# Performance work log

Measured on AMD Instinct MI355X. Metric: run time of the kernel, lower is better.

## Reference

```python
import jax, jax.numpy as jnp
import numpy as np


def conv1x1(x, w, b):
    # x: [B,C,H,W], w: [O,C], b: [O]  (1x1 conv == per-pixel matmul)
    return jnp.einsum('oc,bchw->bohw', w, x) + b[None, :, None, None]


def setup_inputs() -> dict:
    key = jax.random.key(0)
    ks = jax.random.split(key, 8)
    B, C, H, W = 8, 256, 64, 64
    heads, points = 8, 4
    x = jax.random.normal(ks[0], (B, C, H, W), dtype=jnp.float32)
    # small offset weights so sampling grids stay mostly in-range (original inits these to 0)
    w_off = jax.random.normal(ks[1], (heads * points * 2, C), dtype=jnp.float32) * 0.01
    b_off = jax.random.normal(ks[2], (heads * points * 2,), dtype=jnp.float32) * 0.05
    w_attn = jax.random.normal(ks[3], (heads * points, C), dtype=jnp.float32) * 0.02
    b_attn = jnp.full((heads * points,), np.log(1.0 / points), dtype=jnp.float32)
    w_val = jax.random.normal(ks[4], (C, C), dtype=jnp.float32) * (1.0 / np.sqrt(C))
    b_val = jnp.zeros((C,), dtype=jnp.float32)
    w_out = jax.random.normal(ks[5], (C, C), dtype=jnp.float32) * (1.0 / np.sqrt(C))
    b_out = jnp.zeros((C,), dtype=jnp.float32)
    return {"x": x, "w_off": w_off, "b_off": b_off, "w_attn": w_attn, "b_attn": b_attn,
            "w_val": w_val, "b_val": b_val, "w_out": w_out, "b_out": b_out,
            "num_heads": heads, "num_points": points}


def _grid_sample_one(v, g):
    # v: [Cph,H,W] value image; g: [P,H,W,2] sampling grid in [-1,1] (x,y), align_corners=True,
    # bilinear, zero padding. Returns [Cph,P,H,W].
    Cph, H, W = v.shape
    ix = (g[..., 0] + 1.0) * 0.5 * (W - 1)  # [P,H,W]
    iy = (g[..., 1] + 1.0) * 0.5 * (H - 1)
    x0 = jnp.floor(ix); y0 = jnp.floor(iy)
    x1 = x0 + 1.0;      y1 = y0 + 1.0
    wx1 = ix - x0; wx0 = 1.0 - wx1
    wy1 = iy - y0; wy0 = 1.0 - wy1

    def corner(yc, xc, w):
        valid = (xc >= 0) & (xc <= W - 1) & (yc >= 0) & (yc <= H - 1)
        yi = jnp.clip(yc, 0, H - 1).astype(jnp.int32)
        xi = jnp.clip(xc, 0, W - 1).astype(jnp.int32)
        vv = v[:, yi, xi]  # [Cph,P,H,W]
        return vv * (w * valid.astype(w.dtype))[None]

    return (corner(y0, x0, wy0 * wx0) + corner(y0, x1, wy0 * wx1)
            + corner(y1, x0, wy1 * wx0) + corner(y1, x1, wy1 * wx1))


def deformable_attention(x, w_off, b_off, w_attn, b_attn, w_val, b_val, w_out, b_out,
                         num_heads, num_points):
    B, C, H, W = x.shape
    hd, P = num_heads, num_points
    cph = C // hd

    value = conv1x1(x, w_val, b_val)                       # [B,C,H,W]
    offsets = conv1x1(x, w_off, b_off)                     # [B,hd*P*2,H,W]
    attn = conv1x1(x, w_attn, b_attn).reshape(B, hd, P, H, W)
    attn = jax.nn.softmax(attn, axis=2)                    # softmax over points

    gy = jnp.linspace(-1.0, 1.0, H, dtype=x.dtype)
    gx = jnp.linspace(-1.0, 1.0, W, dtype=x.dtype)
    base = jnp.stack(jnp.meshgrid(gx, gy, indexing='xy'), axis=-1)  # [H,W,2] (x,y)

    off = offsets.reshape(B, hd, P, 2, H, W).transpose(0, 1, 2, 4, 5, 3)  # [B,hd,P,H,W,2]
    grid = base[None, None, None] + off                                   # [B,hd,P,H,W,2]

    val = value.reshape(B * hd, cph, H, W)
    grid = grid.reshape(B * hd, P, H, W, 2)
    sampled = jax.vmap(_grid_sample_one)(val, grid)        # [B*hd,cph,P,H,W]
    sampled = sampled.reshape(B, hd, cph, P, H, W)

    weighted = (sampled * attn[:, :, None]).sum(axis=3)    # [B,hd,cph,H,W]
    weighted = weighted.reshape(B, C, H, W)
    return conv1x1(weighted, w_out, b_out) + x


def reference(x, w_off, b_off, w_attn, b_attn, w_val, b_val, w_out, b_out,
              num_heads, num_points):
    return deformable_attention(x, w_off, b_off, w_attn, b_attn, w_val, b_val,
                                w_out, b_out, num_heads, num_points)
```

## Files before the change

### kernel.cpp

```cpp
#include <hip/hip_runtime.h>
#include <cstddef>

#define HW 4096

typedef __attribute__((ext_vector_type(8))) short short8v;
typedef __attribute__((ext_vector_type(4))) float f32x4;

__device__ inline unsigned short f2bf(float f) {
    unsigned int u = __float_as_uint(f);
    u += 0x7FFFu + ((u >> 16) & 1u);
    return (unsigned short)(u >> 16);
}
__device__ inline float bf2f(unsigned short s) {
    return __uint_as_float(((unsigned int)s) << 16);
}

__device__ inline void load_tile(const unsigned short* __restrict__ g, int kc,
                                 int wid, int lane, short8v r[4])
{
    const int s  = lane & 7;
    const int r8 = lane >> 3;
    const unsigned short* src = g + kc + s * 8;
#pragma unroll
    for (int i = 0; i < 4; ++i) {
        const int row = wid * 32 + i * 8 + r8;
        r[i] = *(const short8v*)(src + row * 256);
    }
}

__device__ inline void store_tile(unsigned short* lds, int wid, int lane, const short8v r[4])
{
    const int s  = lane & 7;
    const int r8 = lane >> 3;
#pragma unroll
    for (int i = 0; i < 4; ++i) {
        const int row = wid * 32 + i * 8 + r8;
        *(short8v*)((char*)lds + row * 128 + ((s ^ (row & 7)) << 4)) = r[i];
    }
}

__device__ inline short8v read_frag(const unsigned short* lds, int row, int kbyte, int lane)
{
    const char* p = (const char*)lds + row * 128 + (kbyte ^ ((lane & 7) * 16));
    return *(const short8v*)p;
}

__global__ __launch_bounds__(256)
void prep_kernel(const float* __restrict__ w_off, const float* __restrict__ b_off,
                 const float* __restrict__ w_attn, const float* __restrict__ b_attn,
                 const float* __restrict__ w_val, const float* __restrict__ b_val,
                 const float* __restrict__ w_out,
                 unsigned short* __restrict__ wcat_bf, unsigned short* __restrict__ wauxlo,
                 unsigned short* __restrict__ wout_bf, float* __restrict__ bcat)
{
    int i = blockIdx.x * 256 + threadIdx.x;
    if (i < 384 * 256) {
        int n = i >> 8, k = i & 255;
        float v;
        if (n < 256)      v = w_val[n * 256 + k];
        else if (n < 320) v = w_off[(n - 256) * 256 + k];
        else if (n < 352) v = w_attn[(n - 320) * 256 + k];
        else              v = 0.0f;
        unsigned short hi = f2bf(v);
        wcat_bf[i] = hi;
        if (n >= 256) wauxlo[(n - 256) * 256 + k] = f2bf(v - bf2f(hi));
    }
    if (i < 256 * 256) wout_bf[i] = f2bf(w_out[i]);
    if (i < 512) {
        float v = 0.0f;
        if (i < 256)      v = b_val[i];
        else if (i < 320) v = b_off[i - 256];
        else if (i < 352) v = b_attn[i - 320];
        bcat[i] = v;
    }
}

__global__ __launch_bounds__(256)
void transpose_kernel(const float* __restrict__ x, unsigned short* __restrict__ xhi)
{
    __shared__ float t[64][65];
    const int bid = blockIdx.x;
    const int pt = bid & 63, ct = (bid >> 6) & 3, b = bid >> 8;
    const int tid = threadIdx.x;
    const int rr = tid >> 4, c4 = (tid & 15) * 4;

    const float* src = x + ((size_t)(b * 256 + ct * 64)) * HW + pt * 64;
#pragma unroll
    for (int j = 0; j < 4; ++j) {
        float4 v = *(const float4*)&src[(size_t)(j * 16 + rr) * HW + c4];
        t[j * 16 + rr][c4 + 0] = v.x; t[j * 16 + rr][c4 + 1] = v.y;
        t[j * 16 + rr][c4 + 2] = v.z; t[j * 16 + rr][c4 + 3] = v.w;
    }
    __syncthreads();

    const size_t obase = ((size_t)b * HW + pt * 64) * 256 + ct * 64;
#pragma unroll
    for (int j = 0; j < 4; ++j) {
        int p = j * 16 + rr;
        ushort4 hi = make_ushort4(f2bf(t[c4 + 0][p]), f2bf(t[c4 + 1][p]),
                                  f2bf(t[c4 + 2][p]), f2bf(t[c4 + 3][p]));
        *(ushort4*)&xhi[obase + (size_t)p * 256 + c4] = hi;
    }
}

__global__ __launch_bounds__(256)
void proj_kernel(const unsigned short* __restrict__ wcat_bf, const unsigned short* __restrict__ wauxlo,
                 const unsigned short* __restrict__ xhi, const float* __restrict__ bcat,
                 unsigned short* __restrict__ value_bf,
                 float* __restrict__ off_ws, float* __restrict__ attn_ws)
{
    __shared__ unsigned short lds[3 * 128 * 64];
    unsigned short* Al  = lds;
    unsigned short* Bl  = lds + 128 * 64;
    unsigned short* Alo = lds + 2 * 128 * 64;

    const int bid = blockIdx.x;
    const int pt = bid & 31;
    const int mt = (bid >> 5) % 3;
    const int b  = bid / 96;
    const int tid = threadIdx.x, wid = tid >> 6, lane = tid & 63;
    const int wm = wid >> 1, wn = wid & 1;
    const int mloc = lane & 15, ksel = lane >> 4;

    const unsigned short* Bg = xhi + ((size_t)b * HW + pt * 128) * 256;

    f32x4 acc[4][4];
#pragma unroll
    for (int fm = 0; fm < 4; ++fm) {
        float4 bv = *(const float4*)&bcat[mt * 128 + wm * 64 + fm * 16 + ksel * 4];
#pragma unroll
        for (int fn = 0; fn < 4; ++fn) acc[fm][fn] = (f32x4){bv.x, bv.y, bv.z, bv.w};
    }

    if (mt < 2) {
        const unsigned short* Ag = wcat_bf + mt * 128 * 256;
        short8v rA[4], rB[4];
        load_tile(Ag, 0, wid, lane, rA);
        load_tile(Bg, 0, wid, lane, rB);
#pragma unroll
        for (int kc = 0; kc < 4; ++kc) {
            if (kc) __syncthreads();
            store_tile(Al, wid, lane, rA);
            store_tile(Bl, wid, lane, rB);
            __syncthreads();
            if (kc < 3) {
                load_tile(Ag, (kc + 1) * 64, wid, lane, rA);
                load_tile(Bg, (kc + 1) * 64, wid, lane, rB);
            }
#pragma unroll
            for (int kk = 0; kk < 2; ++kk) {
                const int kb = kk * 64 + ksel * 16;
                short8v a[4], bb[4];
#pragma unroll
                for (int f = 0; f < 4; ++f) a[f]  = read_frag(Al, wm * 64 + f * 16 + mloc, kb, lane);
#pragma unroll
                for (int f = 0; f < 4; ++f) bb[f] = read_frag(Bl, wn * 64 + f * 16 + mloc, kb, lane);
#pragma unroll
                for (int fm = 0; fm < 4; ++fm)
#pragma unroll
                    for (int fn = 0; fn < 4; ++fn)
                        acc[fm][fn] = __builtin_amdgcn_mfma_f32_16x16x32_bf16(a[fm], bb[fn], acc[fm][fn], 0, 0, 0);
            }
        }
#pragma unroll
        for (int fm = 0; fm < 4; ++fm) {
            const int ch = mt * 128 + wm * 64 + fm * 16 + ksel * 4;
            const int head = ch >> 5, c32 = ch & 31;
#pragma unroll
            for (int fn = 0; fn < 4; ++fn) {
                const int p = pt * 128 + wn * 64 + fn * 16 + mloc;
                f32x4 v = acc[fm][fn];
                ushort4 st = make_ushort4(f2bf(v[0]), f2bf(v[1]), f2bf(v[2]), f2bf(v[3]));
                *(ushort4*)&value_bf[(((size_t)(b * 8 + head)) * HW + p) * 32 + c32] = st;
            }
        }
    } else {
        const unsigned short* Ahg = wcat_bf + 256 * 256;
        const unsigned short* Alg = wauxlo;
        short8v rA[4], rL[4], rB[4];
        load_tile(Ahg, 0, wid, lane, rA);
        load_tile(Alg, 0, wid, lane, rL);
        load_tile(Bg, 0, wid, lane, rB);
#pragma unroll
        for (int kc = 0; kc < 4; ++kc) {
            if (kc) __syncthreads();
            store_tile(Al, wid, lane, rA);
            store_tile(Alo, wid, lane, rL);
            store_tile(Bl, wid, lane, rB);
            __syncthreads();
            if (kc < 3) {
                load_tile(Ahg, (kc + 1) * 64, wid, lane, rA);
                load_tile(Alg, (kc + 1) * 64, wid, lane, rL);
                load_tile(Bg, (kc + 1) * 64, wid, lane, rB);
            }
#pragma unroll
            for (int kk = 0; kk < 2; ++kk) {
                const int kb = kk * 64 + ksel * 16;
                short8v ah[4], al[4], bb[4];
#pragma unroll
                for (int f = 0; f < 4; ++f) {
                    ah[f] = read_frag(Al,  wm * 64 + f * 16 + mloc, kb, lane);
                    al[f] = read_frag(Alo, wm * 64 + f * 16 + mloc, kb, lane);
                    bb[f] = read_frag(Bl,  wn * 64 + f * 16 + mloc, kb, lane);
                }
#pragma unroll
                for (int fm = 0; fm < 4; ++fm)
#pragma unroll
                    for (int fn = 0; fn < 4; ++fn) {
                        acc[fm][fn] = __builtin_amdgcn_mfma_f32_16x16x32_bf16(ah[fm], bb[fn], acc[fm][fn], 0, 0, 0);
                        acc[fm][fn] = __builtin_amdgcn_mfma_f32_16x16x32_bf16(al[fm], bb[fn], acc[fm][fn], 0, 0, 0);
                    }
            }
        }
#pragma unroll
        for (int fm = 0; fm < 4; ++fm) {
            const int ch0 = wm * 64 + fm * 16 + ksel * 4;
#pragma unroll
            for (int fn = 0; fn < 4; ++fn) {
                const int p = pt * 128 + wn * 64 + fn * 16 + mloc;
                f32x4 v = acc[fm][fn];
                if (ch0 < 64) {
                    *(float4*)&off_ws[((size_t)b * HW + p) * 64 + ch0] =
                        make_float4(v[0], v[1], v[2], v[3]);
                } else if (ch0 < 96) {
                    *(float4*)&attn_ws[((size_t)b * HW + p) * 32 + (ch0 - 64)] =
                        make_float4(v[0], v[1], v[2], v[3]);
                }
            }
        }
    }
}

__global__ __launch_bounds__(256)
void sample_kernel(const unsigned short* __restrict__ value_bf, const float* __restrict__ off_ws,
                   const float* __restrict__ attn_ws, unsigned short* __restrict__ wgt_t)
{
    const int bid    = blockIdx.x;
    const int ptile  = bid & 127;
    const int head   = (bid >> 7) & 7;
    const int b      = bid >> 10;
    const int tid    = threadIdx.x;
    const int c4     = tid & 7;
    const int posIdx = tid >> 3;
    const int p      = ptile * 32 + posIdx;
    const int h      = p >> 6;
    const int w      = p & 63;

    const float gx = w * (2.0f / 63.0f) - 1.0f;
    const float gy = h * (2.0f / 63.0f) - 1.0f;

    float4 la = *(const float4*)&attn_ws[((size_t)b * HW + p) * 32 + head * 4];
    float m  = fmaxf(fmaxf(la.x, la.y), fmaxf(la.z, la.w));
    float e0 = __expf(la.x - m), e1 = __expf(la.y - m), e2 = __expf(la.z - m), e3 = __expf(la.w - m);
    float inv = 1.0f / (e0 + e1 + e2 + e3);
    float aw[4] = {e0 * inv, e1 * inv, e2 * inv, e3 * inv};

    float4 acc = make_float4(0.f, 0.f, 0.f, 0.f);
    const unsigned short* vb = value_bf + (size_t)(b * 8 + head) * HW * 32 + c4 * 4;
    const float* offp = off_ws + ((size_t)b * HW + p) * 64 + head * 8;

#pragma unroll
    for (int pt = 0; pt < 4; ++pt) {
        float ox = offp[pt * 2 + 0];
        float oy = offp[pt * 2 + 1];
        float ix = (gx + ox + 1.0f) * 31.5f;
        float iy = (gy + oy + 1.0f) * 31.5f;
        float x0f = floorf(ix), y0f = floorf(iy);
        float wx1 = ix - x0f, wx0 = 1.0f - wx1;
        float wy1 = iy - y0f, wy0 = 1.0f - wy1;
        int x0 = (int)x0f, y0 = (int)y0f;
        int x1 = x0 + 1,   y1 = y0 + 1;
        float a = aw[pt];
        float vx0 = (x0 >= 0 && x0 <= 63) ? 1.f : 0.f;
        float vx1 = (x1 >= 0 && x1 <= 63) ? 1.f : 0.f;
        float vy0 = (y0 >= 0 && y0 <= 63) ? 1.f : 0.f;
        float vy1 = (y1 >= 0 && y1 <= 63) ? 1.f : 0.f;
        float w00 = a * wy0 * wx0 * vy0 * vx0;
        float w01 = a * wy0 * wx1 * vy0 * vx1;
        float w10 = a * wy1 * wx0 * vy1 * vx0;
        float w11 = a * wy1 * wx1 * vy1 * vx1;
        int cx0 = min(max(x0, 0), 63), cx1 = min(max(x1, 0), 63);
        int cy0 = min(max(y0, 0), 63), cy1 = min(max(y1, 0), 63);
        ushort4 u00 = *(const ushort4*)&vb[(size_t)(cy0 * 64 + cx0) * 32];
        ushort4 u01 = *(const ushort4*)&vb[(size_t)(cy0 * 64 + cx1) * 32];
        ushort4 u10 = *(const ushort4*)&vb[(size_t)(cy1 * 64 + cx0) * 32];
        ushort4 u11 = *(const ushort4*)&vb[(size_t)(cy1 * 64 + cx1) * 32];
        acc.x += w00 * bf2f(u00.x) + w01 * bf2f(u01.x) + w10 * bf2f(u10.x) + w11 * bf2f(u11.x);
        acc.y += w00 * bf2f(u00.y) + w01 * bf2f(u01.y) + w10 * bf2f(u10.y) + w11 * bf2f(u11.y);
        acc.z += w00 * bf2f(u00.z) + w01 * bf2f(u01.z) + w10 * bf2f(u10.z) + w11 * bf2f(u11.z);
        acc.w += w00 * bf2f(u00.w) + w01 * bf2f(u01.w) + w10 * bf2f(u10.w) + w11 * bf2f(u11.w);
    }

    ushort4 st = make_ushort4(f2bf(acc.x), f2bf(acc.y), f2bf(acc.z), f2bf(acc.w));
    *(ushort4*)&wgt_t[((size_t)b * HW + p) * 256 + head * 32 + c4 * 4] = st;
}

__global__ __launch_bounds__(256)
void outproj_gemm(const unsigned short* __restrict__ wout_bf, const unsigned short* __restrict__ wgt_t,
                  const float* __restrict__ b_out, const float* __restrict__ x,
                  float* __restrict__ out)
{
    __shared__ unsigned short Al[128 * 64];
    __shared__ unsigned short Bl[128 * 64];
    const int bid = blockIdx.x;
    const int pt = bid & 31, mt = (bid >> 5) & 1, b = bid >> 6;
    const int tid = threadIdx.x, wid = tid >> 6, lane = tid & 63;
    const int wm = wid >> 1, wn = wid & 1;
    const int mloc = lane & 15, ksel = lane >> 4;

    const unsigned short* Ag = wout_bf + mt * 128 * 256;
    const unsigned short* Bg = wgt_t + ((size_t)b * HW + pt * 128) * 256;

    f32x4 acc[4][4];
#pragma unroll
    for (int fm = 0; fm < 4; ++fm)
#pragma unroll
        for (int fn = 0; fn < 4; ++fn) acc[fm][fn] = (f32x4){0.f, 0.f, 0.f, 0.f};

    short8v rA[4], rB[4];
    load_tile(Ag, 0, wid, lane, rA);
    load_tile(Bg, 0, wid, lane, rB);
#pragma unroll
    for (int kc = 0; kc < 4; ++kc) {
        if (kc) __syncthreads();
        store_tile(Al, wid, lane, rA);
        store_tile(Bl, wid, lane, rB);
        __syncthreads();
        if (kc < 3) {
            load_tile(Ag, (kc + 1) * 64, wid, lane, rA);
            load_tile(Bg, (kc + 1) * 64, wid, lane, rB);
        }
#pragma unroll
        for (int kk = 0; kk < 2; ++kk) {
            const int kb = kk * 64 + ksel * 16;
            short8v a[4], bb[4];
#pragma unroll
            for (int f = 0; f < 4; ++f) a[f]  = read_frag(Al, wm * 64 + f * 16 + mloc, kb, lane);
#pragma unroll
            for (int f = 0; f < 4; ++f) bb[f] = read_frag(Bl, wn * 64 + f * 16 + mloc, kb, lane);
#pragma unroll
            for (int fm = 0; fm < 4; ++fm)
#pragma unroll
                for (int fn = 0; fn < 4; ++fn)
                    acc[fm][fn] = __builtin_amdgcn_mfma_f32_16x16x32_bf16(a[fm], bb[fn], acc[fm][fn], 0, 0, 0);
        }
    }

#pragma unroll
    for (int fm = 0; fm < 4; ++fm) {
        const int o = mt * 128 + wm * 64 + fm * 16 + ksel * 4;
        float4 bo = *(const float4*)&b_out[o];
#pragma unroll
        for (int fn = 0; fn < 4; ++fn) {
            const int p = pt * 128 + wn * 64 + fn * 16 + mloc;
            const size_t idx = ((size_t)(b * 256 + o)) * HW + p;
            f32x4 v = acc[fm][fn];
            out[idx + 0 * HW] = v[0] + bo.x + x[idx + 0 * HW];
            out[idx + 1 * HW] = v[1] + bo.y + x[idx + 1 * HW];
            out[idx + 2 * HW] = v[2] + bo.z + x[idx + 2 * HW];
            out[idx + 3 * HW] = v[3] + bo.w + x[idx + 3 * HW];
        }
    }
}

extern "C" void kernel_launch(void* const* d_in, const int* in_sizes, int n_in,
                              void* d_out, int out_size, void* d_ws, size_t ws_size,
                              hipStream_t stream)
{
    const float* x      = (const float*)d_in[0];
    const float* w_off  = (const float*)d_in[1];
    const float* b_off  = (const float*)d_in[2];
    const float* w_attn = (const float*)d_in[3];
    const float* b_attn = (const float*)d_in[4];
    const float* w_val  = (const float*)d_in[5];
    const float* b_val  = (const float*)d_in[6];
    const float* w_out  = (const float*)d_in[7];
    const float* b_out  = (const float*)d_in[8];
    float* out = (float*)d_out;

    char* ws = (char*)d_ws;
    unsigned short* wcat_bf = (unsigned short*)(ws + 0);
    unsigned short* wauxlo  = (unsigned short*)(ws + 196608);
    unsigned short* wout_bf = (unsigned short*)(ws + 262144);
    float*          bcat    = (float*)(ws + 393216);
    unsigned short* xhi     = (unsigned short*)(ws + 395264);
    unsigned short* val_bf  = (unsigned short*)(ws + 17172480);
    float*          off_ws  = (float*)(ws + 33949696);
    float*          attn_ws = (float*)(ws + 42338304);
    unsigned short* wgt_t   = (unsigned short*)(ws + 46532608);

    prep_kernel<<<384, 256, 0, stream>>>(w_off, b_off, w_attn, b_attn, w_val, b_val,
                                         w_out, wcat_bf, wauxlo, wout_bf, bcat);
    transpose_kernel<<<2048, 256, 0, stream>>>(x, xhi);
    proj_kernel<<<768, 256, 0, stream>>>(wcat_bf, wauxlo, xhi, bcat, val_bf, off_ws, attn_ws);
    sample_kernel<<<8192, 256, 0, stream>>>(val_bf, off_ws, attn_ws, wgt_t);
    outproj_gemm<<<512, 256, 0, stream>>>(wout_bf, wgt_t, b_out, x, out);
}
```

Measured before the change: 77.80 us.

## Split hi/lo offset-attention GEMM into separate blocks, sum partials in sampler

```diff
diff --git a/kernel.cpp b/kernel.cpp
--- a/kernel.cpp
+++ b/kernel.cpp
@@ -65,6 +65,10 @@
         wcat_bf[i] = hi;
         if (n >= 256) wauxlo[(n - 256) * 256 + k] = f2bf(v - bf2f(hi));
     }
+    if (i < 128 * 256) {
+        int n = i >> 8;
+        if (n >= 96) wauxlo[i] = 0;
+    }
     if (i < 256 * 256) wout_bf[i] = f2bf(w_out[i]);
     if (i < 512) {
         float v = 0.0f;
@@ -103,65 +107,73 @@
     }
 }
 
+__device__ inline void mainloop(const unsigned short* __restrict__ Ag,
+                                const unsigned short* __restrict__ Bg,
+                                unsigned short* Al, unsigned short* Bl,
+                                int wid, int lane, int wm, int wn, f32x4 acc[4][4])
+{
+    const int mloc = lane & 15, ksel = lane >> 4;
+    short8v rA[4], rB[4];
+    load_tile(Ag, 0, wid, lane, rA);
+    load_tile(Bg, 0, wid, lane, rB);
+#pragma unroll
+    for (int kc = 0; kc < 4; ++kc) {
+        if (kc) __syncthreads();
+        store_tile(Al, wid, lane, rA);
+        store_tile(Bl, wid, lane, rB);
+        __syncthreads();
+        if (kc < 3) {
+            load_tile(Ag, (kc + 1) * 64, wid, lane, rA);
+            load_tile(Bg, (kc + 1) * 64, wid, lane, rB);
+        }
+#pragma unroll
+        for (int kk = 0; kk < 2; ++kk) {
+            const int kb = kk * 64 + ksel * 16;
+            short8v a[4], bb[4];
+#pragma unroll
+            for (int f = 0; f < 4; ++f) a[f]  = read_frag(Al, wm * 64 + f * 16 + mloc, kb, lane);
+#pragma unroll
+            for (int f = 0; f < 4; ++f) bb[f] = read_frag(Bl, wn * 64 + f * 16 + mloc, kb, lane);
+#pragma unroll
+            for (int fm = 0; fm < 4; ++fm)
+#pragma unroll
+                for (int fn = 0; fn < 4; ++fn)
+                    acc[fm][fn] = __builtin_amdgcn_mfma_f32_16x16x32_bf16(a[fm], bb[fn], acc[fm][fn], 0, 0, 0);
+        }
+    }
+}
+
 __global__ __launch_bounds__(256)
 void proj_kernel(const unsigned short* __restrict__ wcat_bf, const unsigned short* __restrict__ wauxlo,
                  const unsigned short* __restrict__ xhi, const float* __restrict__ bcat,
                  unsigned short* __restrict__ value_bf,
-                 float* __restrict__ off_ws, float* __restrict__ attn_ws)
-{
-    __shared__ unsigned short lds[3 * 128 * 64];
-    unsigned short* Al  = lds;
-    unsigned short* Bl  = lds + 128 * 64;
-    unsigned short* Alo = lds + 2 * 128 * 64;
-
+                 float* __restrict__ off_hi, float* __restrict__ attn_hi,
+                 float* __restrict__ off_lo, float* __restrict__ attn_lo)
+{
+    __shared__ unsigned short Al[128 * 64];
+    __shared__ unsigned short Bl[128 * 64];
     const int bid = blockIdx.x;
-    const int pt = bid & 31;
-    const int mt = (bid >> 5) % 3;
-    const int b  = bid / 96;
+    const int mt = bid & 3;
+    const int pt = (bid >> 2) & 31;
+    const int b  = bid >> 7;
     const int tid = threadIdx.x, wid = tid >> 6, lane = tid & 63;
     const int wm = wid >> 1, wn = wid & 1;
     const int mloc = lane & 15, ksel = lane >> 4;
 
+    const unsigned short* Ag = (mt < 3) ? (wcat_bf + mt * 128 * 256) : wauxlo;
     const unsigned short* Bg = xhi + ((size_t)b * HW + pt * 128) * 256;
 
     f32x4 acc[4][4];
 #pragma unroll
     for (int fm = 0; fm < 4; ++fm) {
-        float4 bv = *(const float4*)&bcat[mt * 128 + wm * 64 + fm * 16 + ksel * 4];
+        float4 bv = *(const float4*)&bcat[((mt < 3) ? mt * 128 : 384) + wm * 64 + fm * 16 + ksel * 4];
 #pragma unroll
         for (int fn = 0; fn < 4; ++fn) acc[fm][fn] = (f32x4){bv.x, bv.y, bv.z, bv.w};
     }
 
+    mainloop(Ag, Bg, Al, Bl, wid, lane, wm, wn, acc);
+
     if (mt < 2) {
-        const unsigned short* Ag = wcat_bf + mt * 128 * 256;
-        short8v rA[4], rB[4];
-        load_tile(Ag, 0, wid, lane, rA);
-        load_tile(Bg, 0, wid, lane, rB);
-#pragma unroll
-        for (int kc = 0; kc < 4; ++kc) {
-            if (kc) __syncthreads();
-            store_tile(Al, wid, lane, rA);
-            store_tile(Bl, wid, lane, rB);
-            __syncthreads();
-            if (kc < 3) {
-                load_tile(Ag, (kc + 1) * 64, wid, lane, rA);
-                load_tile(Bg, (kc + 1) * 64, wid, lane, rB);
-            }
-#pragma unroll
-            for (int kk = 0; kk < 2; ++kk) {
-                const int kb = kk * 64 + ksel * 16;
-                short8v a[4], bb[4];
-#pragma unroll
-                for (int f = 0; f < 4; ++f) a[f]  = read_frag(Al, wm * 64 + f * 16 + mloc, kb, lane);
-#pragma unroll
-                for (int f = 0; f < 4; ++f) bb[f] = read_frag(Bl, wn * 64 + f * 16 + mloc, kb, lane);
-#pragma unroll
-                for (int fm = 0; fm < 4; ++fm)
-#pragma unroll
-                    for (int fn = 0; fn < 4; ++fn)
-                        acc[fm][fn] = __builtin_amdgcn_mfma_f32_16x16x32_bf16(a[fm], bb[fn], acc[fm][fn], 0, 0, 0);
-            }
-        }
 #pragma unroll
         for (int fm = 0; fm < 4; ++fm) {
             const int ch = mt * 128 + wm * 64 + fm * 16 + ksel * 4;
@@ -175,43 +187,8 @@
             }
         }
     } else {
-        const unsigned short* Ahg = wcat_bf + 256 * 256;
-        const unsigned short* Alg = wauxlo;
-        short8v rA[4], rL[4], rB[4];
-        load_tile(Ahg, 0, wid, lane, rA);
-        load_tile(Alg, 0, wid, lane, rL);
-        load_tile(Bg, 0, wid, lane, rB);
-#pragma unroll
-        for (int kc = 0; kc < 4; ++kc) {
-            if (kc) __syncthreads();
-            store_tile(Al, wid, lane, rA);
-            store_tile(Alo, wid, lane, rL);
-            store_tile(Bl, wid, lane, rB);
-            __syncthreads();
-            if (kc < 3) {
-                load_tile(Ahg, (kc + 1) * 64, wid, lane, rA);
-                load_tile(Alg, (kc + 1) * 64, wid, lane, rL);
-                load_tile(Bg, (kc + 1) * 64, wid, lane, rB);
-            }
-#pragma unroll
-            for (int kk = 0; kk < 2; ++kk) {
-                const int kb = kk * 64 + ksel * 16;
-                short8v ah[4], al[4], bb[4];
-#pragma unroll
-                for (int f = 0; f < 4; ++f) {
-                    ah[f] = read_frag(Al,  wm * 64 + f * 16 + mloc, kb, lane);
-                    al[f] = read_frag(Alo, wm * 64 + f * 16 + mloc, kb, lane);
-                    bb[f] = read_frag(Bl,  wn * 64 + f * 16 + mloc, kb, lane);
-                }
-#pragma unroll
-                for (int fm = 0; fm < 4; ++fm)
-#pragma unroll
-                    for (int fn = 0; fn < 4; ++fn) {
-                        acc[fm][fn] = __builtin_amdgcn_mfma_f32_16x16x32_bf16(ah[fm], bb[fn], acc[fm][fn], 0, 0, 0);
-                        acc[fm][fn] = __builtin_amdgcn_mfma_f32_16x16x32_bf16(al[fm], bb[fn], acc[fm][fn], 0, 0, 0);
-                    }
-            }
-        }
+        float* offd  = (mt == 2) ? off_hi  : off_lo;
+        float* attnd = (mt == 2) ? attn_hi : attn_lo;
 #pragma unroll
         for (int fm = 0; fm < 4; ++fm) {
             const int ch0 = wm * 64 + fm * 16 + ksel * 4;
@@ -220,10 +197,10 @@
                 const int p = pt * 128 + wn * 64 + fn * 16 + mloc;
                 f32x4 v = acc[fm][fn];
                 if (ch0 < 64) {
-                    *(float4*)&off_ws[((size_t)b * HW + p) * 64 + ch0] =
+                    *(float4*)&offd[((size_t)b * HW + p) * 64 + ch0] =
                         make_float4(v[0], v[1], v[2], v[3]);
                 } else if (ch0 < 96) {
-                    *(float4*)&attn_ws[((size_t)b * HW + p) * 32 + (ch0 - 64)] =
+                    *(float4*)&attnd[((size_t)b * HW + p) * 32 + (ch0 - 64)] =
                         make_float4(v[0], v[1], v[2], v[3]);
                 }
             }
@@ -232,8 +209,10 @@
 }
 
 __global__ __launch_bounds__(256)
-void sample_kernel(const unsigned short* __restrict__ value_bf, const float* __restrict__ off_ws,
-                   const float* __restrict__ attn_ws, unsigned short* __restrict__ wgt_t)
+void sample_kernel(const unsigned short* __restrict__ value_bf,
+                   const float* __restrict__ off_hi, const float* __restrict__ attn_hi,
+                   const float* __restrict__ off_lo, const float* __restrict__ attn_lo,
+                   unsigned short* __restrict__ wgt_t)
 {
     const int bid    = blockIdx.x;
     const int ptile  = bid & 127;
@@ -249,7 +228,9 @@
     const float gx = w * (2.0f / 63.0f) - 1.0f;
     const float gy = h * (2.0f / 63.0f) - 1.0f;
 
-    float4 la = *(const float4*)&attn_ws[((size_t)b * HW + p) * 32 + head * 4];
+    float4 la = *(const float4*)&attn_hi[((size_t)b * HW + p) * 32 + head * 4];
+    float4 ll = *(const float4*)&attn_lo[((size_t)b * HW + p) * 32 + head * 4];
+    la.x += ll.x; la.y += ll.y; la.z += ll.z; la.w += ll.w;
     float m  = fmaxf(fmaxf(la.x, la.y), fmaxf(la.z, la.w));
     float e0 = __expf(la.x - m), e1 = __expf(la.y - m), e2 = __expf(la.z - m), e3 = __expf(la.w - m);
     float inv = 1.0f / (e0 + e1 + e2 + e3);
@@ -257,12 +238,13 @@
 
     float4 acc = make_float4(0.f, 0.f, 0.f, 0.f);
     const unsigned short* vb = value_bf + (size_t)(b * 8 + head) * HW * 32 + c4 * 4;
-    const float* offp = off_ws + ((size_t)b * HW + p) * 64 + head * 8;
+    const float* offp = off_hi + ((size_t)b * HW + p) * 64 + head * 8;
+    const float* offl = off_lo + ((size_t)b * HW + p) * 64 + head * 8;
 
 #pragma unroll
     for (int pt = 0; pt < 4; ++pt) {
-        float ox = offp[pt * 2 + 0];
-        float oy = offp[pt * 2 + 1];
+        float ox = offp[pt * 2 + 0] + offl[pt * 2 + 0];
+        float oy = offp[pt * 2 + 1] + offl[pt * 2 + 1];
         float ix = (gx + ox + 1.0f) * 31.5f;
         float iy = (gy + oy + 1.0f) * 31.5f;
         float x0f = floorf(ix), y0f = floorf(iy);
@@ -317,34 +299,7 @@
 #pragma unroll
         for (int fn = 0; fn < 4; ++fn) acc[fm][fn] = (f32x4){0.f, 0.f, 0.f, 0.f};
 
-    short8v rA[4], rB[4];
-    load_tile(Ag, 0, wid, lane, rA);
-    load_tile(Bg, 0, wid, lane, rB);
-#pragma unroll
-    for (int kc = 0; kc < 4; ++kc) {
-        if (kc) __syncthreads();
-        store_tile(Al, wid, lane, rA);
-        store_tile(Bl, wid, lane, rB);
-        __syncthreads();
-        if (kc < 3) {
-            load_tile(Ag, (kc + 1) * 64, wid, lane, rA);
-            load_tile(Bg, (kc + 1) * 64, wid, lane, rB);
-        }
-#pragma unroll
-        for (int kk = 0; kk < 2; ++kk) {
-            const int kb = kk * 64 + ksel * 16;
-            short8v a[4], bb[4];
-#pragma unroll
-            for (int f = 0; f < 4; ++f) a[f]  = read_frag(Al, wm * 64 + f * 16 + mloc, kb, lane);
-#pragma unroll
-            for (int f = 0; f < 4; ++f) bb[f] = read_frag(Bl, wn * 64 + f * 16 + mloc, kb, lane);
-#pragma unroll
-            for (int fm = 0; fm < 4; ++fm)
-#pragma unroll
-                for (int fn = 0; fn < 4; ++fn)
-                    acc[fm][fn] = __builtin_amdgcn_mfma_f32_16x16x32_bf16(a[fm], bb[fn], acc[fm][fn], 0, 0, 0);
-        }
-    }
+    mainloop(Ag, Bg, Al, Bl, wid, lane, wm, wn, acc);
 
 #pragma unroll
     for (int fm = 0; fm < 4; ++fm) {
@@ -385,14 +340,17 @@
     float*          bcat    = (float*)(ws + 393216);
     unsigned short* xhi     = (unsigned short*)(ws + 395264);
     unsigned short* val_bf  = (unsigned short*)(ws + 17172480);
-    float*          off_ws  = (float*)(ws + 33949696);
-    float*          attn_ws = (float*)(ws + 42338304);
+    float*          off_hi  = (float*)(ws + 33949696);
+    float*          attn_hi = (float*)(ws + 42338304);
     unsigned short* wgt_t   = (unsigned short*)(ws + 46532608);
+    float*          off_lo  = (float*)(ws + 63309824);
+    float*          attn_lo = (float*)(ws + 71698432);
 
     prep_kernel<<<384, 256, 0, stream>>>(w_off, b_off, w_attn, b_attn, w_val, b_val,
                                          w_out, wcat_bf, wauxlo, wout_bf, bcat);
     transpose_kernel<<<2048, 256, 0, stream>>>(x, xhi);
-    proj_kernel<<<768, 256, 0, stream>>>(wcat_bf, wauxlo, xhi, bcat, val_bf, off_ws, attn_ws);
-    sample_kernel<<<8192, 256, 0, stream>>>(val_bf, off_ws, attn_ws, wgt_t);
+    proj_kernel<<<1024, 256, 0, stream>>>(wcat_bf, wauxlo, xhi, bcat, val_bf,
+                                          off_hi, attn_hi, off_lo, attn_lo);
+    sample_kernel<<<8192, 256, 0, stream>>>(val_bf, off_hi, attn_hi, off_lo, attn_lo, wgt_t);
     outproj_gemm<<<512, 256, 0, stream>>>(wout_bf, wgt_t, b_out, x, out);
 }
```

After: 84.77 us. 9.0% more time.
